# Kernel optimization log

Hardware: AMD Instinct MI355X
Metric: run time of the kernel (lower is better)

## Reference

```python
import jax, jax.numpy as jnp
import numpy as np


def conv2d(x, w, stride=1, padding=0):
    # x: [N,Ci,H,W], w: [Co,Ci,Kh,Kw]
    return jax.lax.conv_general_dilated(
        x, w, window_strides=(stride, stride),
        padding=[(padding, padding), (padding, padding)],
        dimension_numbers=('NCHW', 'OIHW', 'NCHW'))


def adder2d(x, w, stride=1, padding=0):
    """AdderNet L1-distance conv: out[n,co,ho,wo] = -sum_{ci,kh,kw} |x_patch - w[co,ci,kh,kw]|."""
    N, Ci, H, W = x.shape
    Co, _, K, _ = w.shape
    xp = jnp.pad(x, ((0, 0), (0, 0), (padding, padding), (padding, padding)))
    Ho = (H + 2 * padding - K) // stride + 1
    Wo = (W + 2 * padding - K) // stride + 1
    acc = jnp.zeros((N, Co, Ho, Wo), x.dtype)
    for kh in range(K):  # small fixed loop over kernel taps (<=9)
        for kw in range(K):
            xs = xp[:, :, kh:kh + Ho * stride:stride, kw:kw + Wo * stride:stride]  # [N,Ci,Ho,Wo]
            diff = jnp.abs(xs[:, None] - w[None, :, :, kh, kw, None, None])  # [N,Co,Ci,Ho,Wo]
            acc = acc - diff.sum(axis=2)
    return acc


def batchnorm(x, gamma, beta, mean, var, eps=1e-5):
    inv = gamma / jnp.sqrt(var + eps)
    return x * inv[None, :, None, None] + (beta - mean * inv)[None, :, None, None]


def setup_inputs() -> dict:
    key = jax.random.key(0)
    ks = jax.random.split(key, 16)
    N, C, H, W = 4, 128, 28, 28
    inp = {
        'x': jax.random.normal(ks[0], (N, C, H, W), jnp.float32),
        'w_shift1': jax.random.normal(ks[1], (C, C, 1, 1), jnp.float32) * 0.1,
        'w_add1': jax.random.normal(ks[2], (C, C, 1, 1), jnp.float32) * 0.1,
        'bn1_gamma': jax.random.uniform(ks[3], (C,), jnp.float32, 0.5, 1.5),
        'bn1_beta': jax.random.normal(ks[4], (C,), jnp.float32) * 0.1,
        'bn1_mean': jax.random.normal(ks[5], (C,), jnp.float32),
        'bn1_var': jax.random.uniform(ks[6], (C,), jnp.float32, 0.5, 1.5),
        'w_shift2': jax.random.normal(ks[7], (C, C, 3, 3), jnp.float32) * 0.05,
        'w_add2': jax.random.normal(ks[8], (C, C, 3, 3), jnp.float32) * 0.05,
        'bn2_gamma': jax.random.uniform(ks[9], (C,), jnp.float32, 0.5, 1.5),
        'bn2_beta': jax.random.normal(ks[10], (C,), jnp.float32) * 0.1,
        'bn2_mean': jax.random.normal(ks[11], (C,), jnp.float32),
        'bn2_var': jax.random.uniform(ks[12], (C,), jnp.float32, 0.5, 1.5),
    }
    return inp


def reference(x, w_shift1, w_add1, bn1_gamma, bn1_beta, bn1_mean, bn1_var,
              w_shift2, w_add2, bn2_gamma, bn2_beta, bn2_mean, bn2_var):
    identity = x
    # conv1: 1x1 shift conv -> 1x1 adder
    out = conv2d(x, w_shift1, stride=1, padding=0)
    out = adder2d(out, w_add1, stride=1, padding=0)
    out = jax.nn.relu(batchnorm(out, bn1_gamma, bn1_beta, bn1_mean, bn1_var))
    # conv2: 3x3 shift conv (stride=1, pad=1) -> 3x3 adder (stride=1, pad=1)
    out = conv2d(out, w_shift2, stride=1, padding=1)
    out = adder2d(out, w_add2, stride=1, padding=1)
    out = jax.nn.relu(batchnorm(out, bn2_gamma, bn2_beta, bn2_mean, bn2_var))
    return jax.nn.relu(out + identity)
```

## Files before the change

### kernel.cpp

```cpp
#include <hip/hip_runtime.h>
#include <math.h>

constexpr int C   = 128;
constexpr int HW  = 784;
constexpr int PW  = 32;
constexpr int PH  = 30;
constexpr int PHW = PW * PH;

#define ABS_ACC(acc, d) asm("v_add_f32 %0, %0, abs(%1)" : "+v"(acc) : "v"(d))

__device__ inline void tile_map2(int wg, int& n, int& h0, int& w0) {
    int region = wg & 7;
    int idx    = wg >> 3;
    n = region >> 1;
    int half = region & 1;
    int th = half * 7 + idx / 14;
    int tw = idx % 14;
    h0 = th * 2;
    w0 = tw * 2;
}

__device__ inline void tile_map4(int wg, int& n, int& h0, int& w0, int& co0) {
    int region = wg & 7;
    int rest   = wg >> 3;
    n = region >> 1;
    int half = region & 1;
    co0 = (rest & 1) * 64;
    int idx = rest >> 1;
    int th = idx / 7, tw = idx % 7;
    h0 = half * 14 + th * 2;
    w0 = tw * 4;
}

__device__ inline void zero_border2(float* plane, int h0, int w0) {
    if (h0 == 0) {
        plane[w0 + 1] = 0.f; plane[w0 + 2] = 0.f;
        if (w0 == 0)  plane[0]  = 0.f;
        if (w0 == 26) plane[29] = 0.f;
    }
    if (h0 == 26) {
        plane[29 * PW + w0 + 1] = 0.f; plane[29 * PW + w0 + 2] = 0.f;
        if (w0 == 0)  plane[29 * PW]      = 0.f;
        if (w0 == 26) plane[29 * PW + 29] = 0.f;
    }
    if (w0 == 0)  { plane[(h0 + 1) * PW]      = 0.f; plane[(h0 + 2) * PW]      = 0.f; }
    if (w0 == 26) { plane[(h0 + 1) * PW + 29] = 0.f; plane[(h0 + 2) * PW + 29] = 0.f; }
}

__device__ inline void zero_border4(float* plane, int h0, int w0) {
    if (h0 == 0) {
#pragma unroll
        for (int c = 0; c < 4; ++c) plane[w0 + 1 + c] = 0.f;
        if (w0 == 0)  plane[0]  = 0.f;
        if (w0 == 24) plane[29] = 0.f;
    }
    if (h0 == 26) {
#pragma unroll
        for (int c = 0; c < 4; ++c) plane[29 * PW + w0 + 1 + c] = 0.f;
        if (w0 == 0)  plane[29 * PW]      = 0.f;
        if (w0 == 24) plane[29 * PW + 29] = 0.f;
    }
    if (w0 == 0)  { plane[(h0 + 1) * PW]      = 0.f; plane[(h0 + 2) * PW]      = 0.f; }
    if (w0 == 24) { plane[(h0 + 1) * PW + 29] = 0.f; plane[(h0 + 2) * PW + 29] = 0.f; }
}

__device__ __forceinline__ void loadw9(const float* __restrict__ wb, int ci, float wk[9]) {
    const float* wp = wb + ci * 9 * C;
#pragma unroll
    for (int k = 0; k < 9; ++k) wk[k] = wp[k * C];
}

__device__ __forceinline__ void loadx46(const float* __restrict__ sp0, int ci,
                                        float4 rr[4], float2 ss[4]) {
    const float* sp = sp0 + ci * PHW;
#pragma unroll
    for (int r = 0; r < 4; ++r) {
        rr[r] = *reinterpret_cast<const float4*>(sp + r * PW);
        ss[r] = *reinterpret_cast<const float2*>(sp + r * PW + 4);
    }
}

__device__ __forceinline__ void body_conv(const float wk[9], const float4 rr[4],
                                          const float2 ss[4], float acc[2][4]) {
    float xr[4][6];
#pragma unroll
    for (int r = 0; r < 4; ++r) {
        xr[r][0] = rr[r].x; xr[r][1] = rr[r].y; xr[r][2] = rr[r].z;
        xr[r][3] = rr[r].w; xr[r][4] = ss[r].x; xr[r][5] = ss[r].y;
    }
#pragma unroll
    for (int kh = 0; kh < 3; ++kh)
#pragma unroll
        for (int kw = 0; kw < 3; ++kw) {
            float wv = wk[kh * 3 + kw];
#pragma unroll
            for (int pr = 0; pr < 2; ++pr)
#pragma unroll
                for (int pc = 0; pc < 4; ++pc)
                    acc[pr][pc] = fmaf(xr[pr + kh][pc + kw], wv, acc[pr][pc]);
        }
}

__device__ __forceinline__ void body_adder(const float wk[9], const float4 rr[4],
                                           const float2 ss[4], float acc[2][4]) {
    float xr[4][6];
#pragma unroll
    for (int r = 0; r < 4; ++r) {
        xr[r][0] = rr[r].x; xr[r][1] = rr[r].y; xr[r][2] = rr[r].z;
        xr[r][3] = rr[r].w; xr[r][4] = ss[r].x; xr[r][5] = ss[r].y;
    }
#pragma unroll
    for (int kh = 0; kh < 3; ++kh)
#pragma unroll
        for (int kw = 0; kw < 3; ++kw) {
            float wv = wk[kh * 3 + kw];
#pragma unroll
            for (int pr = 0; pr < 2; ++pr)
#pragma unroll
                for (int pc = 0; pc < 4; ++pc) {
                    float e = xr[pr + kh][pc + kw] - wv;
                    ABS_ACC(acc[pr][pc], e);
                }
        }
}

__global__ __launch_bounds__(256) void reorder_w(const float* __restrict__ w2,
                                                 const float* __restrict__ a2,
                                                 const float* __restrict__ w1,
                                                 const float* __restrict__ a1,
                                                 float* __restrict__ w2r,
                                                 float* __restrict__ a2r,
                                                 float* __restrict__ w1r,
                                                 float* __restrict__ a1r) {
    int idx = blockIdx.x * 256 + threadIdx.x;
    const int T9 = C * C * 9;
    const int T1 = C * C;
    if (idx < 2 * T9) {
        const float* src = w2; float* dst = w2r;
        if (idx >= T9) { idx -= T9; src = a2; dst = a2r; }
        int co = idx & 127;
        int r  = idx >> 7;
        int k  = r % 9;
        int ci = r / 9;
        dst[idx] = src[(co * C + ci) * 9 + k];
        return;
    }
    idx -= 2 * T9;
    if (idx >= 2 * T1) return;
    const float* src = w1; float* dst = w1r;
    if (idx >= T1) { idx -= T1; src = a1; dst = a1r; }
    int co = idx & 127;
    int ci = idx >> 7;
    dst[idx] = src[co * C + ci];
}

__global__ __launch_bounds__(256, 8) void stage1(const float* __restrict__ x,
                                                 const float* __restrict__ w1r,
                                                 const float* __restrict__ a1r,
                                                 const float* __restrict__ g1,
                                                 const float* __restrict__ b1,
                                                 const float* __restrict__ m1,
                                                 const float* __restrict__ v1,
                                                 float* __restrict__ t1p) {
    __shared__ float Xs[C][4];
    __shared__ float Ys[C][4];
    __shared__ float Rs[C][4];
    int n, h0, w0;
    tile_map2(blockIdx.x, n, h0, w0);
    int t   = threadIdx.x;
    int co  = t & 127;
    int ciq = t >> 7;
    int ci0 = ciq * 64;

#pragma unroll
    for (int e = t; e < 512; e += 256) {
        int ci = e >> 2, p = e & 3, r = p >> 1, c = p & 1;
        Xs[ci][p] = x[(n * C + ci) * HW + (h0 + r) * 28 + w0 + c];
    }
    __syncthreads();

    float4 a = make_float4(0.f, 0.f, 0.f, 0.f);
    const float* wp = w1r + co;
#pragma unroll 4
    for (int i = 0; i < 64; ++i) {
        int ci = ci0 + i;
        float wv = wp[ci * C];
        float4 xv = *reinterpret_cast<const float4*>(&Xs[ci][0]);
        a.x = fmaf(xv.x, wv, a.x);
        a.y = fmaf(xv.y, wv, a.y);
        a.z = fmaf(xv.z, wv, a.z);
        a.w = fmaf(xv.w, wv, a.w);
    }
    if (ciq) *reinterpret_cast<float4*>(&Rs[co][0]) = a;
    __syncthreads();
    if (ciq == 0) {
        float4 r = *reinterpret_cast<const float4*>(&Rs[co][0]);
        a.x += r.x; a.y += r.y; a.z += r.z; a.w += r.w;
        *reinterpret_cast<float4*>(&Ys[co][0]) = a;
    }
    __syncthreads();

    float d0 = 0.f, d1 = 0.f, d2 = 0.f, d3 = 0.f;
    const float* ap = a1r + co;
#pragma unroll 4
    for (int i = 0; i < 64; ++i) {
        int ci = ci0 + i;
        float av = ap[ci * C];
        float4 yv = *reinterpret_cast<const float4*>(&Ys[ci][0]);
        float e0 = yv.x - av; ABS_ACC(d0, e0);
        float e1 = yv.y - av; ABS_ACC(d1, e1);
        float e2 = yv.z - av; ABS_ACC(d2, e2);
        float e3 = yv.w - av; ABS_ACC(d3, e3);
    }
    if (ciq) *reinterpret_cast<float4*>(&Rs[co][0]) = make_float4(d0, d1, d2, d3);
    __syncthreads();
    if (ciq == 0) {
        float4 r = *reinterpret_cast<const float4*>(&Rs[co][0]);
        d0 += r.x; d1 += r.y; d2 += r.z; d3 += r.w;
        float inv = g1[co] / sqrtf(v1[co] + 1e-5f);
        float off = b1[co] - m1[co] * inv;
        float* plane = t1p + (n * C + co) * PHW;
        float* dst = plane + (h0 + 1) * PW + (w0 + 1);
        dst[0]      = fmaxf(-d0 * inv + off, 0.f);
        dst[1]      = fmaxf(-d1 * inv + off, 0.f);
        dst[PW + 0] = fmaxf(-d2 * inv + off, 0.f);
        dst[PW + 1] = fmaxf(-d3 * inv + off, 0.f);
        zero_border2(plane, h0, w0);
    }
}

__global__ __launch_bounds__(256, 4) void conv3x3(const float* __restrict__ t1p,
                                                  const float* __restrict__ w2r,
                                                  float* __restrict__ t2p) {
    __shared__ float Rs[3][64][8];
    int n, h0, w0, co0;
    tile_map4(blockIdx.x, n, h0, w0, co0);
    int t   = threadIdx.x;
    int col = t & 63;
    int co  = co0 + col;
    int ciq = t >> 6;
    int ci0u = __builtin_amdgcn_readfirstlane(ciq * 32);

    const float* sp0 = t1p + n * C * PHW + h0 * PW + w0;
    const float* wb  = w2r + co;
    float acc[2][4] = {{0.f,0.f,0.f,0.f},{0.f,0.f,0.f,0.f}};

    float  wkA[9], wkB[9];
    float4 rA[4], rB[4];
    float2 sA[4], sB[4];

    loadw9(wb, ci0u, wkA);
    loadx46(sp0, ci0u, rA, sA);
#pragma unroll 1
    for (int i = 0; i < 32; i += 2) {
        int ciB = ci0u + i + 1;
        loadw9(wb, ciB, wkB);
        loadx46(sp0, ciB, rB, sB);
        body_conv(wkA, rA, sA, acc);
        int ciA = ci0u + ((i + 2) & 31);
        loadw9(wb, ciA, wkA);
        loadx46(sp0, ciA, rA, sA);
        body_conv(wkB, rB, sB, acc);
    }

    if (ciq) {
        *reinterpret_cast<float4*>(&Rs[ciq - 1][col][0]) = make_float4(acc[0][0], acc[0][1], acc[0][2], acc[0][3]);
        *reinterpret_cast<float4*>(&Rs[ciq - 1][col][4]) = make_float4(acc[1][0], acc[1][1], acc[1][2], acc[1][3]);
    }
    __syncthreads();
    if (ciq == 0) {
#pragma unroll
        for (int q = 0; q < 3; ++q) {
            float4 r0 = *reinterpret_cast<const float4*>(&Rs[q][col][0]);
            float4 r1 = *reinterpret_cast<const float4*>(&Rs[q][col][4]);
            acc[0][0] += r0.x; acc[0][1] += r0.y; acc[0][2] += r0.z; acc[0][3] += r0.w;
            acc[1][0] += r1.x; acc[1][1] += r1.y; acc[1][2] += r1.z; acc[1][3] += r1.w;
        }
        float* plane = t2p + (n * C + co) * PHW;
        float* dst = plane + (h0 + 1) * PW + (w0 + 1);
#pragma unroll
        for (int pc = 0; pc < 4; ++pc) dst[pc]      = acc[0][pc];
#pragma unroll
        for (int pc = 0; pc < 4; ++pc) dst[PW + pc] = acc[1][pc];
        zero_border4(plane, h0, w0);
    }
}

__global__ __launch_bounds__(256, 4) void adder3x3(const float* __restrict__ t2p,
                                                   const float* __restrict__ a2r,
                                                   const float* __restrict__ x0,
                                                   const float* __restrict__ g2,
                                                   const float* __restrict__ b2,
                                                   const float* __restrict__ m2,
                                                   const float* __restrict__ v2,
                                                   float* __restrict__ out) {
    __shared__ float Rs[3][64][8];
    int n, h0, w0, co0;
    tile_map4(blockIdx.x, n, h0, w0, co0);
    int t   = threadIdx.x;
    int col = t & 63;
    int co  = co0 + col;
    int ciq = t >> 6;
    int ci0u = __builtin_amdgcn_readfirstlane(ciq * 32);

    const float* sp0 = t2p + n * C * PHW + h0 * PW + w0;
    const float* wb  = a2r + co;
    float acc[2][4] = {{0.f,0.f,0.f,0.f},{0.f,0.f,0.f,0.f}};

    float  wkA[9], wkB[9];
    float4 rA[4], rB[4];
    float2 sA[4], sB[4];

    loadw9(wb, ci0u, wkA);
    loadx46(sp0, ci0u, rA, sA);
#pragma unroll 1
    for (int i = 0; i < 32; i += 2) {
        int ciB = ci0u + i + 1;
        loadw9(wb, ciB, wkB);
        loadx46(sp0, ciB, rB, sB);
        body_adder(wkA, rA, sA, acc);
        int ciA = ci0u + ((i + 2) & 31);
        loadw9(wb, ciA, wkA);
        loadx46(sp0, ciA, rA, sA);
        body_adder(wkB, rB, sB, acc);
    }

    if (ciq) {
        *reinterpret_cast<float4*>(&Rs[ciq - 1][col][0]) = make_float4(acc[0][0], acc[0][1], acc[0][2], acc[0][3]);
        *reinterpret_cast<float4*>(&Rs[ciq - 1][col][4]) = make_float4(acc[1][0], acc[1][1], acc[1][2], acc[1][3]);
    }
    __syncthreads();
    if (ciq == 0) {
#pragma unroll
        for (int q = 0; q < 3; ++q) {
            float4 r0 = *reinterpret_cast<const float4*>(&Rs[q][col][0]);
            float4 r1 = *reinterpret_cast<const float4*>(&Rs[q][col][4]);
            acc[0][0] += r0.x; acc[0][1] += r0.y; acc[0][2] += r0.z; acc[0][3] += r0.w;
            acc[1][0] += r1.x; acc[1][1] += r1.y; acc[1][2] += r1.z; acc[1][3] += r1.w;
        }
        float inv = g2[co] / sqrtf(v2[co] + 1e-5f);
        float off = b2[co] - m2[co] * inv;
        int base = (n * C + co) * HW + h0 * 28 + w0;
#pragma unroll
        for (int pr = 0; pr < 2; ++pr) {
#pragma unroll
            for (int pc = 0; pc < 4; ++pc) {
                float z = fmaxf(-acc[pr][pc] * inv + off, 0.f);
                z += x0[base + pr * 28 + pc];
                out[base + pr * 28 + pc] = fmaxf(z, 0.f);
            }
        }
    }
}

extern "C" void kernel_launch(void* const* d_in, const int* in_sizes, int n_in,
                              void* d_out, int out_size, void* d_ws, size_t ws_size,
                              hipStream_t stream) {
    const float* x   = (const float*)d_in[0];
    const float* w1  = (const float*)d_in[1];
    const float* a1  = (const float*)d_in[2];
    const float* g1  = (const float*)d_in[3];
    const float* b1  = (const float*)d_in[4];
    const float* m1  = (const float*)d_in[5];
    const float* v1  = (const float*)d_in[6];
    const float* w2  = (const float*)d_in[7];
    const float* a2  = (const float*)d_in[8];
    const float* g2  = (const float*)d_in[9];
    const float* b2  = (const float*)d_in[10];
    const float* m2  = (const float*)d_in[11];
    const float* v2  = (const float*)d_in[12];
    float* out = (float*)d_out;

    float* ws  = (float*)d_ws;
    float* t1p = ws;
    float* t2p = t1p + 4 * C * PHW;
    float* w2r = t2p + 4 * C * PHW;
    float* a2r = w2r + C * C * 9;
    float* w1r = a2r + C * C * 9;
    float* a1r = w1r + C * C;

    const int reorder_total = 2 * C * C * 9 + 2 * C * C;
    reorder_w<<<(reorder_total + 255) / 256, 256, 0, stream>>>(w2, a2, w1, a1, w2r, a2r, w1r, a1r);
    stage1<<<784, 256, 0, stream>>>(x, w1r, a1r, g1, b1, m1, v1, t1p);
    conv3x3<<<784, 256, 0, stream>>>(t1p, w2r, t2p);
    adder3x3<<<784, 256, 0, stream>>>(t2p, a2r, x, g2, b2, m2, v2, out);
}
```

Measured before the change: 69.85 us.

## Stage 3x3 weights via global_load_lds double-buffered LDS in conv and adder

Replaces per-thread register loads of the nine weight taps with direct global-to-LDS DMA (global_load_lds), double-buffered across input channels, and reads weights back from LDS. The input tile loads are no longer software-prefetched into registers; they are now issued in the same iteration they are consumed. The aim is to cut VGPR pressure and vector load latency for weights, at the cost of extra LDS traffic, losing the x prefetch overlap, and relying on a hand-written vmcnt wait. There is no barrier between waves, but each wave writes and reads only its own LDS slice, so this looks safe.

```diff
diff --git a/kernel.cpp b/kernel.cpp
--- a/kernel.cpp
+++ b/kernel.cpp
@@ -64,12 +64,6 @@
     if (w0 == 24) { plane[(h0 + 1) * PW + 29] = 0.f; plane[(h0 + 2) * PW + 29] = 0.f; }
 }
 
-__device__ __forceinline__ void loadw9(const float* __restrict__ wb, int ci, float wk[9]) {
-    const float* wp = wb + ci * 9 * C;
-#pragma unroll
-    for (int k = 0; k < 9; ++k) wk[k] = wp[k * C];
-}
-
 __device__ __forceinline__ void loadx46(const float* __restrict__ sp0, int ci,
                                         float4 rr[4], float2 ss[4]) {
     const float* sp = sp0 + ci * PHW;
@@ -122,6 +116,12 @@
                     ABS_ACC(acc[pr][pc], e);
                 }
         }
+}
+
+__device__ __forceinline__ void dma_w_row(const float* gp_lane, float* lds_row) {
+    __builtin_amdgcn_global_load_lds(
+        (const __attribute__((address_space(1))) void*)(const void*)gp_lane,
+        (__attribute__((address_space(3))) void*)lds_row, 4, 0, 0);
 }
 
 __global__ __launch_bounds__(256) void reorder_w(const float* __restrict__ w2,
@@ -233,6 +233,7 @@
                                                   const float* __restrict__ w2r,
                                                   float* __restrict__ t2p) {
     __shared__ float Rs[3][64][8];
+    __shared__ float Wl[2][4][9][64];
     int n, h0, w0, co0;
     tile_map4(blockIdx.x, n, h0, w0, co0);
     int t   = threadIdx.x;
@@ -241,26 +242,28 @@
     int ciq = t >> 6;
     int ci0u = __builtin_amdgcn_readfirstlane(ciq * 32);
 
-    const float* sp0 = t1p + n * C * PHW + h0 * PW + w0;
-    const float* wb  = w2r + co;
+    const float* sp0  = t1p + n * C * PHW + h0 * PW + w0;
+    const float* wsrc = w2r + co0 + col;
     float acc[2][4] = {{0.f,0.f,0.f,0.f},{0.f,0.f,0.f,0.f}};
 
-    float  wkA[9], wkB[9];
-    float4 rA[4], rB[4];
-    float2 sA[4], sB[4];
-
-    loadw9(wb, ci0u, wkA);
-    loadx46(sp0, ci0u, rA, sA);
+#pragma unroll
+    for (int k = 0; k < 9; ++k)
+        dma_w_row(wsrc + (ci0u * 9 + k) * C, &Wl[0][ciq][k][0]);
+
 #pragma unroll 1
-    for (int i = 0; i < 32; i += 2) {
-        int ciB = ci0u + i + 1;
-        loadw9(wb, ciB, wkB);
-        loadx46(sp0, ciB, rB, sB);
-        body_conv(wkA, rA, sA, acc);
-        int ciA = ci0u + ((i + 2) & 31);
-        loadw9(wb, ciA, wkA);
-        loadx46(sp0, ciA, rA, sA);
-        body_conv(wkB, rB, sB, acc);
+    for (int i = 0; i < 32; ++i) {
+        int cin = ci0u + ((i + 1) & 31);
+        int bn  = (i + 1) & 1;
+#pragma unroll
+        for (int k = 0; k < 9; ++k)
+            dma_w_row(wsrc + (cin * 9 + k) * C, &Wl[bn][ciq][k][0]);
+        asm volatile("s_waitcnt vmcnt(9)" ::: "memory");
+        float wk[9];
+#pragma unroll
+        for (int k = 0; k < 9; ++k) wk[k] = Wl[i & 1][ciq][k][col];
+        float4 rr[4]; float2 ss[4];
+        loadx46(sp0, ci0u + i, rr, ss);
+        body_conv(wk, rr, ss, acc);
     }
 
     if (ciq) {
@@ -295,6 +298,7 @@
                                                    const float* __restrict__ v2,
                                                    float* __restrict__ out) {
     __shared__ float Rs[3][64][8];
+    __shared__ float Wl[2][4][9][64];
     int n, h0, w0, co0;
     tile_map4(blockIdx.x, n, h0, w0, co0);
     int t   = threadIdx.x;
@@ -303,26 +307,28 @@
     int ciq = t >> 6;
     int ci0u = __builtin_amdgcn_readfirstlane(ciq * 32);
 
-    const float* sp0 = t2p + n * C * PHW + h0 * PW + w0;
-    const float* wb  = a2r + co;
+    const float* sp0  = t2p + n * C * PHW + h0 * PW + w0;
+    const float* wsrc = a2r + co0 + col;
     float acc[2][4] = {{0.f,0.f,0.f,0.f},{0.f,0.f,0.f,0.f}};
 
-    float  wkA[9], wkB[9];
-    float4 rA[4], rB[4];
-    float2 sA[4], sB[4];
-
-    loadw9(wb, ci0u, wkA);
-    loadx46(sp0, ci0u, rA, sA);
+#pragma unroll
+    for (int k = 0; k < 9; ++k)
+        dma_w_row(wsrc + (ci0u * 9 + k) * C, &Wl[0][ciq][k][0]);
+
 #pragma unroll 1
-    for (int i = 0; i < 32; i += 2) {
-        int ciB = ci0u + i + 1;
-        loadw9(wb, ciB, wkB);
-        loadx46(sp0, ciB, rB, sB);
-        body_adder(wkA, rA, sA, acc);
-        int ciA = ci0u + ((i + 2) & 31);
-        loadw9(wb, ciA, wkA);
-        loadx46(sp0, ciA, rA, sA);
-        body_adder(wkB, rB, sB, acc);
+    for (int i = 0; i < 32; ++i) {
+        int cin = ci0u + ((i + 1) & 31);
+        int bn  = (i + 1) & 1;
+#pragma unroll
+        for (int k = 0; k < 9; ++k)
+            dma_w_row(wsrc + (cin * 9 + k) * C, &Wl[bn][ciq][k][0]);
+        asm volatile("s_waitcnt vmcnt(9)" ::: "memory");
+        float wk[9];
+#pragma unroll
+        for (int k = 0; k < 9; ++k) wk[k] = Wl[i & 1][ciq][k][col];
+        float4 rr[4]; float2 ss[4];
+        loadx46(sp0, ci0u + i, rr, ss);
+        body_adder(wk, rr, ss, acc);
     }
 
     if (ciq) {
```

Result: slower. 90.33 us (+29.3%).
